# Kernel tuning notes

Hardware: AMD Instinct MI355X
Metric: run time of the kernel (lower is better)

## Reference

```python
import jax, jax.numpy as jnp
import numpy as np

N_NODES = 50000
N_EDGES = 800000
V_IN, V_OUT, E_IN, E_OUT = 128, 64, 64, 64


def setup_inputs() -> dict:
    key = jax.random.key(0)
    ks = jax.random.split(key, 9)
    return {
        "n_feat": jax.random.normal(ks[0], (N_NODES, V_IN), dtype=jnp.float32),
        "e_feat": jax.random.normal(ks[1], (N_EDGES, E_IN), dtype=jnp.float32),
        "src": jax.random.randint(ks[2], (N_EDGES,), 0, N_NODES),
        "dst": jax.random.randint(ks[3], (N_EDGES,), 0, N_NODES),
        "W_a": jax.random.normal(ks[4], (2 * V_IN + E_IN, V_OUT), dtype=jnp.float32) * 0.1,
        "W_T": jax.random.normal(ks[5], (2 * V_IN + E_IN, V_OUT), dtype=jnp.float32) * 0.1,
        "b_T": jnp.zeros((V_OUT,), dtype=jnp.float32),
        "W_e": jax.random.normal(ks[6], (V_IN, E_OUT), dtype=jnp.float32) * 0.1,
        "W_ee": jax.random.normal(ks[7], (E_IN, E_OUT), dtype=jnp.float32) * 0.1,
        "prelu_a": jnp.full((1,), 0.25, dtype=jnp.float32),
    }


def _prelu(x, a):
    return jnp.where(x >= 0, x, a * x)


def reference(n_feat, e_feat, src, dst, W_a, W_T, b_T, W_e, W_ee, prelu_a):
    v, e_in = V_IN, E_IN
    Ns = n_feat[src]            # [E, v_in] gathered source feats
    Nd = n_feat[dst]            # [E, v_in] gathered dest feats
    # concat order in message_function is [N_dst, e, N_src]; split weights instead of
    # materializing the [E, 2v+e] concat.
    Wa_d, Wa_e, Wa_s = W_a[:v], W_a[v:v + e_in], W_a[v + e_in:]
    Wt_d, Wt_e, Wt_s = W_T[:v], W_T[v:v + e_in], W_T[v + e_in:]
    logits = _prelu(Nd @ Wa_d + e_feat @ Wa_e + Ns @ Wa_s, prelu_a)   # [E, v_out]
    unatt = Nd @ Wt_d + e_feat @ Wt_e + Ns @ Wt_s                      # [E, v_out]
    # ragged per-dst-node softmax over incoming-edge mailbox, per feature channel
    m = jax.ops.segment_max(logits, dst, num_segments=N_NODES)         # [N, v_out]
    m = jnp.where(jnp.isfinite(m), m, 0.0)
    ex = jnp.exp(logits - m[dst])                                      # [E, v_out]
    denom = jax.ops.segment_sum(ex, dst, num_segments=N_NODES)         # [N, v_out]
    num = jax.ops.segment_sum(ex * unatt, dst, num_segments=N_NODES)   # [N, v_out]
    deg = jax.ops.segment_sum(jnp.ones((dst.shape[0],), jnp.float32), dst, num_segments=N_NODES)
    has_msg = (deg > 0)[:, None]
    denom_safe = jnp.where(has_msg, denom, 1.0)
    # DGL leaves 0-in-degree nodes at zeros (reduce never called for them)
    new_n_feat = jnp.where(has_msg, num / denom_safe + b_T, 0.0)       # [N, v_out]
    # edge update uses the OLD node features (apply_edges runs before n_feat swap)
    new_e_feat = Ns @ W_e + Nd @ W_e + e_feat @ W_ee                   # [E, e_out]
    return new_n_feat, new_e_feat
```

## Files before the change

### kernel.cpp

```cpp
#include <hip/hip_runtime.h>

#define N_NODES 50000
#define N_EDGES 800000

typedef __attribute__((ext_vector_type(8))) short short8;
typedef __attribute__((ext_vector_type(4))) float f32x4;

__device__ __forceinline__ short bf16_rne(float f) {
  unsigned u = __float_as_uint(f);
  unsigned r = (u + 0x7FFFu + ((u >> 16) & 1u)) >> 16;
  return (short)r;
}

__global__ __launch_bounds__(256) void prep_w(
    const float* __restrict__ W_a, const float* __restrict__ W_T,
    const float* __restrict__ W_e, unsigned short* __restrict__ Wbf) {
  int t = blockIdx.x * 256 + threadIdx.x;
  if (t >= 4 * 20 * 64 * 8) return;
  int kt = t / 10240, rdm = t % 10240;
  int ct = rdm >> 9, L = (rdm >> 3) & 63, j = rdm & 7;
  int k = kt * 32 + (L >> 4) * 8 + j;
  int oc = ct * 16 + (L & 15);
  float v;
  if (oc < 64)       v = W_a[k * 64 + oc];
  else if (oc < 128) v = W_e[k * 64 + (oc - 64)];
  else if (oc < 192) v = W_a[(192 + k) * 64 + (oc - 128)];
  else if (oc < 256) v = W_T[(192 + k) * 64 + (oc - 192)];
  else               v = W_T[k * 64 + (oc - 256)];
  Wbf[t] = (unsigned short)bf16_rne(v);
}

__global__ __launch_bounds__(256) void hist_kernel(
    const int* __restrict__ dst, unsigned* __restrict__ hist) {
  int e = blockIdx.x * 256 + threadIdx.x;
  if (e < N_EDGES) atomicAdd(&hist[dst[e]], 1u);
}

__global__ __launch_bounds__(1024) void scan_cursor(
    const unsigned* __restrict__ hist, unsigned* __restrict__ cursor) {
  __shared__ unsigned sSums[16];
  const int tid = threadIdx.x;
  const int lane = tid & 63;
  const int w = tid >> 6;
  const int CH = (N_NODES + 1023) / 1024;
  const int begin = tid * CH;
  const int end = (begin + CH < N_NODES) ? begin + CH : N_NODES;

  unsigned local = 0;
  for (int i = begin; i < end; ++i) local += hist[i];

  unsigned sum = local;
  #pragma unroll
  for (int off = 1; off < 64; off <<= 1) {
    unsigned t = __shfl_up(sum, off, 64);
    if (lane >= off) sum += t;
  }
  if (lane == 63) sSums[w] = sum;
  __syncthreads();
  if (w == 0) {
    unsigned v = (lane < 16) ? sSums[lane] : 0u;
    unsigned s2 = v;
    #pragma unroll
    for (int off = 1; off < 16; off <<= 1) {
      unsigned t = __shfl_up(s2, off, 64);
      if (lane >= off) s2 += t;
    }
    if (lane < 16) sSums[lane] = s2 - v;
  }
  __syncthreads();

  unsigned run = sSums[w] + (sum - local);
  for (int i = begin; i < end; ++i) {
    cursor[i] = run;
    run += hist[i];
  }
}

__global__ __launch_bounds__(256) void scatter_kernel(
    const int* __restrict__ src, const int* __restrict__ dst,
    unsigned* __restrict__ cursor, int* __restrict__ perm,
    int* __restrict__ ssrc, int* __restrict__ sdst) {
  int e = blockIdx.x * 256 + threadIdx.x;
  if (e >= N_EDGES) return;
  int d = dst[e];
  unsigned pos = atomicAdd(&cursor[d], 1u);
  perm[pos] = e;
  ssrc[pos] = src[e];
  sdst[pos] = d;
}

__global__ __launch_bounds__(256) void node_proj_mfma(
    const float* __restrict__ n_feat, const unsigned short* __restrict__ Wbf,
    uint2* __restrict__ NPs4, float* __restrict__ Ptd) {
  __shared__ short sA[64 * 128];
  const int tid = threadIdx.x;
  const int lane = tid & 63;
  const int wid = tid >> 6;
  const int n0 = blockIdx.x * 64;

  for (int cid = tid; cid < 64 * 16; cid += 256) {
    int nd = cid >> 4, k8 = cid & 15;
    int nsrc = n0 + nd; if (nsrc >= N_NODES) nsrc = N_NODES - 1;
    const float* p = n_feat + (size_t)nsrc * 128 + k8 * 8;
    float4 v0 = *(const float4*)p;
    float4 v1 = *(const float4*)(p + 4);
    short8 a;
    a[0] = bf16_rne(v0.x); a[1] = bf16_rne(v0.y);
    a[2] = bf16_rne(v0.z); a[3] = bf16_rne(v0.w);
    a[4] = bf16_rne(v1.x); a[5] = bf16_rne(v1.y);
    a[6] = bf16_rne(v1.z); a[7] = bf16_rne(v1.w);
    *(short8*)(&sA[nd * 128 + ((k8 ^ (nd & 7)) << 3)]) = a;
  }
  __syncthreads();

  const int row = lane & 15;
  const int q   = lane >> 4;

  short8 afrag[4];
  #pragma unroll
  for (int kt = 0; kt < 4; ++kt) {
    int nd = wid * 16 + row;
    afrag[kt] = *(const short8*)(&sA[nd * 128 + (((kt * 4 + q) ^ (row & 7)) << 3)]);
  }

  const short8* Wb8 = (const short8*)Wbf;
  f32x4 acc[20];
  #pragma unroll
  for (int ct = 0; ct < 20; ++ct) acc[ct] = (f32x4){0.f, 0.f, 0.f, 0.f};
  #pragma unroll
  for (int ct = 0; ct < 20; ++ct)
    #pragma unroll
    for (int kt = 0; kt < 4; ++kt) {
      short8 b = Wb8[(kt * 20 + ct) * 64 + lane];
      acc[ct] = __builtin_amdgcn_mfma_f32_16x16x32_bf16(afrag[kt], b, acc[ct], 0, 0, 0);
    }

  #pragma unroll
  for (int i = 0; i < 4; ++i)
    #pragma unroll
    for (int r = 0; r < 4; ++r) {
      int nd = n0 + wid * 16 + q * 4 + r;
      if (nd < N_NODES) {
        unsigned e16  = (unsigned short)bf16_rne(acc[4  + i][r]);
        unsigned as16 = (unsigned short)bf16_rne(acc[8  + i][r]);
        unsigned ts16 = (unsigned short)bf16_rne(acc[12 + i][r]);
        unsigned ad16 = (unsigned short)bf16_rne(acc[i][r]);
        uint2 v;
        v.x = e16 | (as16 << 16);
        v.y = ts16 | (ad16 << 16);
        NPs4[(size_t)nd * 64 + i * 16 + row] = v;
        Ptd[(size_t)nd * 64 + i * 16 + row] = acc[16 + i][r];
      }
    }
}

__global__ __launch_bounds__(256) void edge_pass_mfma(
    const float* __restrict__ e_feat, const int* __restrict__ perm,
    const int* __restrict__ ssrc, const int* __restrict__ sdst,
    const float* __restrict__ W_a, const float* __restrict__ W_T,
    const float* __restrict__ W_ee, const float* __restrict__ prelu_a,
    const uint2* __restrict__ NPs4,
    float* __restrict__ denom, float* __restrict__ numer,
    float* __restrict__ out_e) {
  __shared__ short sWT[192 * 64];
  __shared__ float sAcc[4][4 * 200];
  const int tid = threadIdx.x;
  const int lane = tid & 63;
  const int wid = tid >> 6;

  for (int idx = tid; idx < 192 * 32; idx += 256) {
    int C = idx >> 5;
    int k = (idx & 31) * 2;
    float f0, f1;
    if (C < 64)       { f0 = W_a[(128 + k) * 64 + C];        f1 = W_a[(129 + k) * 64 + C]; }
    else if (C < 128) { f0 = W_T[(128 + k) * 64 + (C - 64)]; f1 = W_T[(129 + k) * 64 + (C - 64)]; }
    else              { f0 = W_ee[k * 64 + (C - 128)];       f1 = W_ee[(k + 1) * 64 + (C - 128)]; }
    unsigned pack = ((unsigned)(unsigned short)bf16_rne(f0)) |
                    (((unsigned)(unsigned short)bf16_rne(f1)) << 16);
    int sidx = C * 64 + (((k >> 3) ^ (C & 7)) << 3) + (k & 7);
    *(unsigned*)(&sWT[sidx]) = pack;
  }
  __syncthreads();
  const float pa = prelu_a[0];

  const int row = lane & 15;
  const int q   = lane >> 4;
  float* sA = sAcc[wid];

  const int ngroups = N_EDGES / 64;
  for (int g = blockIdx.x; g < ngroups; g += gridDim.x) {
    const int ebase = g * 64 + wid * 16;

    const int sv = ssrc[ebase + row];
    const int dv = sdst[ebase + row];
    const int pv = perm[ebase + row];

    const float* pbase = e_feat + (size_t)pv * 64;
    float4 v00 = *(const float4*)(pbase + q * 8);
    float4 v01 = *(const float4*)(pbase + q * 8 + 4);
    float4 v10 = *(const float4*)(pbase + 32 + q * 8);
    float4 v11 = *(const float4*)(pbase + 32 + q * 8 + 4);

    uint2 ps[16];
    #pragma unroll
    for (int m = 0; m < 16; ++m) {
      int s_m = __builtin_amdgcn_readlane(sv, m);
      ps[m] = NPs4[(size_t)s_m * 64 + lane];
    }

    short8 afrag[2];
    {
      short8 a;
      a[0] = bf16_rne(v00.x); a[1] = bf16_rne(v00.y);
      a[2] = bf16_rne(v00.z); a[3] = bf16_rne(v00.w);
      a[4] = bf16_rne(v01.x); a[5] = bf16_rne(v01.y);
      a[6] = bf16_rne(v01.z); a[7] = bf16_rne(v01.w);
      afrag[0] = a;
      a[0] = bf16_rne(v10.x); a[1] = bf16_rne(v10.y);
      a[2] = bf16_rne(v10.z); a[3] = bf16_rne(v10.w);
      a[4] = bf16_rne(v11.x); a[5] = bf16_rne(v11.y);
      a[6] = bf16_rne(v11.z); a[7] = bf16_rne(v11.w);
      afrag[1] = a;
    }

    f32x4 aa[4], at[4], ae[4];
    #pragma unroll
    for (int ct = 0; ct < 4; ++ct) {
      aa[ct] = (f32x4){0.f, 0.f, 0.f, 0.f};
      at[ct] = (f32x4){0.f, 0.f, 0.f, 0.f};
      ae[ct] = (f32x4){0.f, 0.f, 0.f, 0.f};
    }
    #pragma unroll
    for (int kt = 0; kt < 2; ++kt)
      #pragma unroll
      for (int ct = 0; ct < 4; ++ct) {
        int c = ct * 16 + row;
        int kg = ((kt * 4 + q) ^ (c & 7)) << 3;
        short8 ba = *(const short8*)(&sWT[(c)       * 64 + kg]);
        short8 bt = *(const short8*)(&sWT[(64 + c)  * 64 + kg]);
        short8 be = *(const short8*)(&sWT[(128 + c) * 64 + kg]);
        aa[ct] = __builtin_amdgcn_mfma_f32_16x16x32_bf16(afrag[kt], ba, aa[ct], 0, 0, 0);
        at[ct] = __builtin_amdgcn_mfma_f32_16x16x32_bf16(afrag[kt], bt, at[ct], 0, 0, 0);
        ae[ct] = __builtin_amdgcn_mfma_f32_16x16x32_bf16(afrag[kt], be, ae[ct], 0, 0, 0);
      }

    int dA = -1, dB = -1;
    float dsA = 0.f, nsA = 0.f, eA = 0.f, adA = 0.f;
    float dsB = 0.f, nsB = 0.f, eB = 0.f, adB = 0.f;

    #pragma unroll
    for (int r = 0; r < 4; ++r) {
      #pragma unroll
      for (int ct = 0; ct < 4; ++ct) {
        sA[q * 200 +       ct * 16 + row] = aa[ct][r];
        sA[q * 200 +  64 + ct * 16 + row] = at[ct][r];
        sA[q * 200 + 128 + ct * 16 + row] = ae[ct][r];
      }
      #pragma unroll
      for (int j = 0; j < 4; ++j) {
        const int m = j * 4 + r;
        int d  = __builtin_amdgcn_readlane(dv, m);
        int eo = __builtin_amdgcn_readlane(pv, m);
        float e_s  = __uint_as_float(ps[m].x << 16);
        float as_s = __uint_as_float(ps[m].x & 0xFFFF0000u);
        float ts_s = __uint_as_float(ps[m].y << 16);
        float aaE = sA[j * 200 + lane];
        float atE = sA[j * 200 + 64 + lane];
        float aeE = sA[j * 200 + 128 + lane];

        float e_d, ad_d;
        bool inA;
        if (d == dA) { e_d = eA; ad_d = adA; inA = true; }
        else if (d == dB) { e_d = eB; ad_d = adB; inA = false; }
        else {
          uint2 pdv = NPs4[(size_t)d * 64 + lane];
          e_d  = __uint_as_float(pdv.x << 16);
          ad_d = __uint_as_float(pdv.y & 0xFFFF0000u);
          if (dA < 0) { dA = d; dsA = 0.f; nsA = 0.f; eA = e_d; adA = ad_d; inA = true; }
          else {
            if (dB >= 0) {
              atomicAdd(denom + (size_t)dB * 64 + lane, dsB);
              atomicAdd(numer + (size_t)dB * 64 + lane, nsB);
            }
            dB = d; dsB = 0.f; nsB = 0.f; eB = e_d; adB = ad_d; inA = false;
          }
        }

        float la = ad_d + aaE + as_s;
        float lg = la >= 0.f ? la : pa * la;
        float ex = __expf(lg);
        float exun = ex * (atE + ts_s);
        out_e[(size_t)eo * 64 + lane] = e_s + e_d + aeE;

        if (inA) { dsA += ex; nsA += exun; }
        else     { dsB += ex; nsB += exun; }
      }
    }
    if (dA >= 0) {
      atomicAdd(denom + (size_t)dA * 64 + lane, dsA);
      atomicAdd(numer + (size_t)dA * 64 + lane, nsA);
    }
    if (dB >= 0) {
      atomicAdd(denom + (size_t)dB * 64 + lane, dsB);
      atomicAdd(numer + (size_t)dB * 64 + lane, nsB);
    }
  }
}

__global__ __launch_bounds__(256) void node_final(
    const float* __restrict__ denom, const float* __restrict__ numer,
    const float* __restrict__ Ptd, const float* __restrict__ b_T,
    float* __restrict__ out_n) {
  int t = blockIdx.x * 256 + threadIdx.x;
  if (t >= N_NODES * 64) return;
  float dn = denom[t];
  out_n[t] = dn > 0.f ? numer[t] / dn + Ptd[t] + b_T[t & 63] : 0.f;
}

extern "C" void kernel_launch(void* const* d_in, const int* in_sizes, int n_in,
                              void* d_out, int out_size, void* d_ws, size_t ws_size,
                              hipStream_t stream) {
  const float* n_feat  = (const float*)d_in[0];
  const float* e_feat  = (const float*)d_in[1];
  const int*   src     = (const int*)d_in[2];
  const int*   dst     = (const int*)d_in[3];
  const float* W_a     = (const float*)d_in[4];
  const float* W_T     = (const float*)d_in[5];
  const float* b_T     = (const float*)d_in[6];
  const float* W_e     = (const float*)d_in[7];
  const float* W_ee    = (const float*)d_in[8];
  const float* prelu_a = (const float*)d_in[9];

  float* out_n = (float*)d_out;
  float* out_e = out_n + (size_t)N_NODES * 64;

  uint2* NPs4  = (uint2*)d_ws;
  float* Ptd   = (float*)((char*)d_ws + (size_t)N_NODES * 64 * 8);
  float* denom = Ptd + (size_t)N_NODES * 64;
  float* numer = denom + (size_t)N_NODES * 64;
  unsigned short* Wbf = (unsigned short*)(numer + (size_t)N_NODES * 64);
  unsigned* hist   = (unsigned*)(Wbf + 40960);
  unsigned* cursor = hist + N_NODES;
  int* perm = (int*)(cursor + N_NODES);
  int* ssrc = perm + N_EDGES;
  int* sdst = ssrc + N_EDGES;

  hipMemsetAsync(denom, 0, (size_t)N_NODES * 64 * 2 * sizeof(float), stream);
  hipMemsetAsync(hist, 0, (size_t)N_NODES * sizeof(unsigned), stream);

  prep_w<<<160, 256, 0, stream>>>(W_a, W_T, W_e, Wbf);
  hist_kernel<<<(N_EDGES + 255) / 256, 256, 0, stream>>>(dst, hist);
  scan_cursor<<<1, 1024, 0, stream>>>(hist, cursor);
  scatter_kernel<<<(N_EDGES + 255) / 256, 256, 0, stream>>>(src, dst, cursor,
                                                            perm, ssrc, sdst);
  node_proj_mfma<<<(N_NODES + 63) / 64, 256, 0, stream>>>(n_feat, Wbf, NPs4, Ptd);
  edge_pass_mfma<<<2048, 256, 0, stream>>>(e_feat, perm, ssrc, sdst, W_a, W_T,
                                           W_ee, prelu_a, NPs4, denom, numer, out_e);
  node_final<<<(N_NODES * 64 + 255) / 256, 256, 0, stream>>>(denom, numer, Ptd, b_T, out_n);
}
```

Baseline: 424.4 us.

## Process edges per destination node in CSR order, removing atomics and node_final

The edge pass now iterates per destination node: each wave handles one node's CSR edge range in chunks of 16, accumulates the softmax denominator and numerator in registers, and writes the final node output directly. This removes the denom/numer memset, the float atomics, and the separate node_final kernel. It also merges the histogram and weight-prep kernels and packs src and edge id into one int2 array. In exchange, nodes with degree not divisible by 16 leave MFMA lanes partly idle, and per-wave work varies with node degree, which can cause load imbalance.

```diff
diff --git a/kernel.cpp b/kernel.cpp
--- a/kernel.cpp
+++ b/kernel.cpp
@@ -12,32 +12,34 @@
   return (short)r;
 }
 
-__global__ __launch_bounds__(256) void prep_w(
+__global__ __launch_bounds__(256) void hist_prep(
+    const int* __restrict__ dst, unsigned* __restrict__ hist,
     const float* __restrict__ W_a, const float* __restrict__ W_T,
     const float* __restrict__ W_e, unsigned short* __restrict__ Wbf) {
-  int t = blockIdx.x * 256 + threadIdx.x;
-  if (t >= 4 * 20 * 64 * 8) return;
-  int kt = t / 10240, rdm = t % 10240;
-  int ct = rdm >> 9, L = (rdm >> 3) & 63, j = rdm & 7;
-  int k = kt * 32 + (L >> 4) * 8 + j;
-  int oc = ct * 16 + (L & 15);
-  float v;
-  if (oc < 64)       v = W_a[k * 64 + oc];
-  else if (oc < 128) v = W_e[k * 64 + (oc - 64)];
-  else if (oc < 192) v = W_a[(192 + k) * 64 + (oc - 128)];
-  else if (oc < 256) v = W_T[(192 + k) * 64 + (oc - 192)];
-  else               v = W_T[k * 64 + (oc - 256)];
-  Wbf[t] = (unsigned short)bf16_rne(v);
-}
-
-__global__ __launch_bounds__(256) void hist_kernel(
-    const int* __restrict__ dst, unsigned* __restrict__ hist) {
-  int e = blockIdx.x * 256 + threadIdx.x;
-  if (e < N_EDGES) atomicAdd(&hist[dst[e]], 1u);
+  const int bid = blockIdx.x;
+  if (bid < N_EDGES / 256) {
+    int e = bid * 256 + threadIdx.x;
+    atomicAdd(&hist[dst[e]], 1u);
+  } else {
+    int t = (bid - N_EDGES / 256) * 256 + threadIdx.x;
+    if (t >= 4 * 20 * 64 * 8) return;
+    int kt = t / 10240, rdm = t % 10240;
+    int ct = rdm >> 9, L = (rdm >> 3) & 63, j = rdm & 7;
+    int k = kt * 32 + (L >> 4) * 8 + j;
+    int oc = ct * 16 + (L & 15);
+    float v;
+    if (oc < 64)       v = W_a[k * 64 + oc];
+    else if (oc < 128) v = W_e[k * 64 + (oc - 64)];
+    else if (oc < 192) v = W_a[(192 + k) * 64 + (oc - 128)];
+    else if (oc < 256) v = W_T[(192 + k) * 64 + (oc - 192)];
+    else               v = W_T[k * 64 + (oc - 256)];
+    Wbf[t] = (unsigned short)bf16_rne(v);
+  }
 }
 
 __global__ __launch_bounds__(1024) void scan_cursor(
-    const unsigned* __restrict__ hist, unsigned* __restrict__ cursor) {
+    const unsigned* __restrict__ hist, unsigned* __restrict__ cursor,
+    unsigned* __restrict__ rowptr) {
   __shared__ unsigned sSums[16];
   const int tid = threadIdx.x;
   const int lane = tid & 63;
@@ -72,21 +74,20 @@
   unsigned run = sSums[w] + (sum - local);
   for (int i = begin; i < end; ++i) {
     cursor[i] = run;
+    rowptr[i] = run;
     run += hist[i];
   }
+  if (tid == 0) rowptr[N_NODES] = N_EDGES;
 }
 
 __global__ __launch_bounds__(256) void scatter_kernel(
     const int* __restrict__ src, const int* __restrict__ dst,
-    unsigned* __restrict__ cursor, int* __restrict__ perm,
-    int* __restrict__ ssrc, int* __restrict__ sdst) {
+    unsigned* __restrict__ cursor, int2* __restrict__ se) {
   int e = blockIdx.x * 256 + threadIdx.x;
   if (e >= N_EDGES) return;
   int d = dst[e];
   unsigned pos = atomicAdd(&cursor[d], 1u);
-  perm[pos] = e;
-  ssrc[pos] = src[e];
-  sdst[pos] = d;
+  se[pos] = make_int2(src[e], e);
 }
 
 __global__ __launch_bounds__(256) void node_proj_mfma(
@@ -154,14 +155,14 @@
     }
 }
 
-__global__ __launch_bounds__(256) void edge_pass_mfma(
-    const float* __restrict__ e_feat, const int* __restrict__ perm,
-    const int* __restrict__ ssrc, const int* __restrict__ sdst,
+__global__ __launch_bounds__(256) void edge_node_pass(
+    const float* __restrict__ e_feat, const int2* __restrict__ se,
+    const unsigned* __restrict__ rowptr,
     const float* __restrict__ W_a, const float* __restrict__ W_T,
     const float* __restrict__ W_ee, const float* __restrict__ prelu_a,
-    const uint2* __restrict__ NPs4,
-    float* __restrict__ denom, float* __restrict__ numer,
-    float* __restrict__ out_e) {
+    const uint2* __restrict__ NPs4, const float* __restrict__ Ptd,
+    const float* __restrict__ b_T,
+    float* __restrict__ out_n, float* __restrict__ out_e) {
   __shared__ short sWT[192 * 64];
   __shared__ float sAcc[4][4 * 200];
   const int tid = threadIdx.x;
@@ -182,139 +183,112 @@
   }
   __syncthreads();
   const float pa = prelu_a[0];
+  const float bT = b_T[lane];
 
   const int row = lane & 15;
   const int q   = lane >> 4;
   float* sA = sAcc[wid];
-
-  const int ngroups = N_EDGES / 64;
-  for (int g = blockIdx.x; g < ngroups; g += gridDim.x) {
-    const int ebase = g * 64 + wid * 16;
-
-    const int sv = ssrc[ebase + row];
-    const int dv = sdst[ebase + row];
-    const int pv = perm[ebase + row];
-
-    const float* pbase = e_feat + (size_t)pv * 64;
-    float4 v00 = *(const float4*)(pbase + q * 8);
-    float4 v01 = *(const float4*)(pbase + q * 8 + 4);
-    float4 v10 = *(const float4*)(pbase + 32 + q * 8);
-    float4 v11 = *(const float4*)(pbase + 32 + q * 8 + 4);
-
-    uint2 ps[16];
-    #pragma unroll
-    for (int m = 0; m < 16; ++m) {
-      int s_m = __builtin_amdgcn_readlane(sv, m);
-      ps[m] = NPs4[(size_t)s_m * 64 + lane];
-    }
-
-    short8 afrag[2];
-    {
-      short8 a;
-      a[0] = bf16_rne(v00.x); a[1] = bf16_rne(v00.y);
-      a[2] = bf16_rne(v00.z); a[3] = bf16_rne(v00.w);
-      a[4] = bf16_rne(v01.x); a[5] = bf16_rne(v01.y);
-      a[6] = bf16_rne(v01.z); a[7] = bf16_rne(v01.w);
-      afrag[0] = a;
-      a[0] = bf16_rne(v10.x); a[1] = bf16_rne(v10.y);
-      a[2] = bf16_rne(v10.z); a[3] = bf16_rne(v10.w);
-      a[4] = bf16_rne(v11.x); a[5] = bf16_rne(v11.y);
-      a[6] = bf16_rne(v11.z); a[7] = bf16_rne(v11.w);
-      afrag[1] = a;
-    }
-
-    f32x4 aa[4], at[4], ae[4];
-    #pragma unroll
-    for (int ct = 0; ct < 4; ++ct) {
-      aa[ct] = (f32x4){0.f, 0.f, 0.f, 0.f};
-      at[ct] = (f32x4){0.f, 0.f, 0.f, 0.f};
-      ae[ct] = (f32x4){0.f, 0.f, 0.f, 0.f};
-    }
-    #pragma unroll
-    for (int kt = 0; kt < 2; ++kt)
+  const int nwaves = gridDim.x * 4;
+
+  for (int n = blockIdx.x * 4 + wid; n < N_NODES; n += nwaves) {
+    const unsigned base = rowptr[n];
+    const int deg = (int)(rowptr[n + 1] - base);
+
+    uint2 pdv = NPs4[(size_t)n * 64 + lane];
+    float e_d  = __uint_as_float(pdv.x << 16);
+    float ad_d = __uint_as_float(pdv.y & 0xFFFF0000u);
+
+    float dsum = 0.f, nsum = 0.f;
+
+    for (int b = 0; b < deg; b += 16) {
+      int cnt = deg - b; if (cnt > 16) cnt = 16;
+      int rslot = (int)base + b + (row < cnt ? row : 0);
+      int2 se2 = se[rslot];
+
+      const float* pbase = e_feat + (size_t)se2.y * 64;
+      float4 v00 = *(const float4*)(pbase + q * 8);
+      float4 v01 = *(const float4*)(pbase + q * 8 + 4);
+      float4 v10 = *(const float4*)(pbase + 32 + q * 8);
+      float4 v11 = *(const float4*)(pbase + 32 + q * 8 + 4);
+
+      uint2 ps[16];
+      #pragma unroll
+      for (int m = 0; m < 16; ++m) {
+        if (m < cnt) {
+          int s_m = __builtin_amdgcn_readlane(se2.x, m);
+          ps[m] = NPs4[(size_t)s_m * 64 + lane];
+        }
+      }
+
+      short8 afrag[2];
+      {
+        short8 a;
+        a[0] = bf16_rne(v00.x); a[1] = bf16_rne(v00.y);
+        a[2] = bf16_rne(v00.z); a[3] = bf16_rne(v00.w);
+        a[4] = bf16_rne(v01.x); a[5] = bf16_rne(v01.y);
+        a[6] = bf16_rne(v01.z); a[7] = bf16_rne(v01.w);
+        afrag[0] = a;
+        a[0] = bf16_rne(v10.x); a[1] = bf16_rne(v10.y);
+        a[2] = bf16_rne(v10.z); a[3] = bf16_rne(v10.w);
+        a[4] = bf16_rne(v11.x); a[5] = bf16_rne(v11.y);
+        a[6] = bf16_rne(v11.z); a[7] = bf16_rne(v11.w);
+        afrag[1] = a;
+      }
+
+      f32x4 aa[4], at[4], ae[4];
       #pragma unroll
       for (int ct = 0; ct < 4; ++ct) {
-        int c = ct * 16 + row;
-        int kg = ((kt * 4 + q) ^ (c & 7)) << 3;
-        short8 ba = *(const short8*)(&sWT[(c)       * 64 + kg]);
-        short8 bt = *(const short8*)(&sWT[(64 + c)  * 64 + kg]);
-        short8 be = *(const short8*)(&sWT[(128 + c) * 64 + kg]);
-        aa[ct] = __builtin_amdgcn_mfma_f32_16x16x32_bf16(afrag[kt], ba, aa[ct], 0, 0, 0);
-        at[ct] = __builtin_amdgcn_mfma_f32_16x16x32_bf16(afrag[kt], bt, at[ct], 0, 0, 0);
-        ae[ct] = __builtin_amdgcn_mfma_f32_16x16x32_bf16(afrag[kt], be, ae[ct], 0, 0, 0);
-      }
-
-    int dA = -1, dB = -1;
-    float dsA = 0.f, nsA = 0.f, eA = 0.f, adA = 0.f;
-    float dsB = 0.f, nsB = 0.f, eB = 0.f, adB = 0.f;
-
-    #pragma unroll
-    for (int r = 0; r < 4; ++r) {
+        aa[ct] = (f32x4){0.f, 0.f, 0.f, 0.f};
+        at[ct] = (f32x4){0.f, 0.f, 0.f, 0.f};
+        ae[ct] = (f32x4){0.f, 0.f, 0.f, 0.f};
+      }
       #pragma unroll
-      for (int ct = 0; ct < 4; ++ct) {
-        sA[q * 200 +       ct * 16 + row] = aa[ct][r];
-        sA[q * 200 +  64 + ct * 16 + row] = at[ct][r];
-        sA[q * 200 + 128 + ct * 16 + row] = ae[ct][r];
-      }
+      for (int kt = 0; kt < 2; ++kt)
+        #pragma unroll
+        for (int ct = 0; ct < 4; ++ct) {
+          int c = ct * 16 + row;
+          int kg = ((kt * 4 + q) ^ (c & 7)) << 3;
+          short8 ba = *(const short8*)(&sWT[(c)       * 64 + kg]);
+          short8 bt = *(const short8*)(&sWT[(64 + c)  * 64 + kg]);
+          short8 be = *(const short8*)(&sWT[(128 + c) * 64 + kg]);
+          aa[ct] = __builtin_amdgcn_mfma_f32_16x16x32_bf16(afrag[kt], ba, aa[ct], 0, 0, 0);
+          at[ct] = __builtin_amdgcn_mfma_f32_16x16x32_bf16(afrag[kt], bt, at[ct], 0, 0, 0);
+          ae[ct] = __builtin_amdgcn_mfma_f32_16x16x32_bf16(afrag[kt], be, ae[ct], 0, 0, 0);
+        }
+
       #pragma unroll
-      for (int j = 0; j < 4; ++j) {
-        const int m = j * 4 + r;
-        int d  = __builtin_amdgcn_readlane(dv, m);
-        int eo = __builtin_amdgcn_readlane(pv, m);
-        float e_s  = __uint_as_float(ps[m].x << 16);
-        float as_s = __uint_as_float(ps[m].x & 0xFFFF0000u);
-        float ts_s = __uint_as_float(ps[m].y << 16);
-        float aaE = sA[j * 200 + lane];
-        float atE = sA[j * 200 + 64 + lane];
-        float aeE = sA[j * 200 + 128 + lane];
-
-        float e_d, ad_d;
-        bool inA;
-        if (d == dA) { e_d = eA; ad_d = adA; inA = true; }
-        else if (d == dB) { e_d = eB; ad_d = adB; inA = false; }
-        else {
-          uint2 pdv = NPs4[(size_t)d * 64 + lane];
-          e_d  = __uint_as_float(pdv.x << 16);
-          ad_d = __uint_as_float(pdv.y & 0xFFFF0000u);
-          if (dA < 0) { dA = d; dsA = 0.f; nsA = 0.f; eA = e_d; adA = ad_d; inA = true; }
-          else {
-            if (dB >= 0) {
-              atomicAdd(denom + (size_t)dB * 64 + lane, dsB);
-              atomicAdd(numer + (size_t)dB * 64 + lane, nsB);
-            }
-            dB = d; dsB = 0.f; nsB = 0.f; eB = e_d; adB = ad_d; inA = false;
+      for (int r = 0; r < 4; ++r) {
+        #pragma unroll
+        for (int ct = 0; ct < 4; ++ct) {
+          sA[q * 200 +       ct * 16 + row] = aa[ct][r];
+          sA[q * 200 +  64 + ct * 16 + row] = at[ct][r];
+          sA[q * 200 + 128 + ct * 16 + row] = ae[ct][r];
+        }
+        #pragma unroll
+        for (int j2 = 0; j2 < 4; ++j2) {
+          const int m = j2 * 4 + r;
+          if (m < cnt) {
+            int eo = __builtin_amdgcn_readlane(se2.y, m);
+            float e_s  = __uint_as_float(ps[m].x << 16);
+            float as_s = __uint_as_float(ps[m].x & 0xFFFF0000u);
+            float ts_s = __uint_as_float(ps[m].y << 16);
+            float aaE = sA[j2 * 200 + lane];
+            float atE = sA[j2 * 200 + 64 + lane];
+            float aeE = sA[j2 * 200 + 128 + lane];
+            float la = ad_d + aaE + as_s;
+            float lg = la >= 0.f ? la : pa * la;
+            float ex = __expf(lg);
+            nsum = __builtin_fmaf(ex, atE + ts_s, nsum);
+            dsum += ex;
+            out_e[(size_t)eo * 64 + lane] = e_s + e_d + aeE;
           }
         }
-
-        float la = ad_d + aaE + as_s;
-        float lg = la >= 0.f ? la : pa * la;
-        float ex = __expf(lg);
-        float exun = ex * (atE + ts_s);
-        out_e[(size_t)eo * 64 + lane] = e_s + e_d + aeE;
-
-        if (inA) { dsA += ex; nsA += exun; }
-        else     { dsB += ex; nsB += exun; }
       }
     }
-    if (dA >= 0) {
-      atomicAdd(denom + (size_t)dA * 64 + lane, dsA);
-      atomicAdd(numer + (size_t)dA * 64 + lane, nsA);
-    }
-    if (dB >= 0) {
-      atomicAdd(denom + (size_t)dB * 64 + lane, dsB);
-      atomicAdd(numer + (size_t)dB * 64 + lane, nsB);
-    }
-  }
-}
-
-__global__ __launch_bounds__(256) void node_final(
-    const float* __restrict__ denom, const float* __restrict__ numer,
-    const float* __restrict__ Ptd, const float* __restrict__ b_T,
-    float* __restrict__ out_n) {
-  int t = blockIdx.x * 256 + threadIdx.x;
-  if (t >= N_NODES * 64) return;
-  float dn = denom[t];
-  out_n[t] = dn > 0.f ? numer[t] / dn + Ptd[t] + b_T[t & 63] : 0.f;
+
+    out_n[(size_t)n * 64 + lane] =
+        deg > 0 ? nsum / dsum + Ptd[(size_t)n * 64 + lane] + bT : 0.f;
+  }
 }
 
 extern "C" void kernel_launch(void* const* d_in, const int* in_sizes, int n_in,
@@ -336,25 +310,17 @@
 
   uint2* NPs4  = (uint2*)d_ws;
   float* Ptd   = (float*)((char*)d_ws + (size_t)N_NODES * 64 * 8);
-  float* denom = Ptd + (size_t)N_NODES * 64;
-  float* numer = denom + (size_t)N_NODES * 64;
-  unsigned short* Wbf = (unsigned short*)(numer + (size_t)N_NODES * 64);
+  unsigned short* Wbf = (unsigned short*)(Ptd + (size_t)N_NODES * 64);
   unsigned* hist   = (unsigned*)(Wbf + 40960);
   unsigned* cursor = hist + N_NODES;
-  int* perm = (int*)(cursor + N_NODES);
-  int* ssrc = perm + N_EDGES;
-  int* sdst = ssrc + N_EDGES;
-
-  hipMemsetAsync(denom, 0, (size_t)N_NODES * 64 * 2 * sizeof(float), stream);
+  unsigned* rowptr = cursor + N_NODES;
+  int2* se = (int2*)(rowptr + N_NODES + 2);
+
   hipMemsetAsync(hist, 0, (size_t)N_NODES * sizeof(unsigned), stream);
-
-  prep_w<<<160, 256, 0, stream>>>(W_a, W_T, W_e, Wbf);
-  hist_kernel<<<(N_EDGES + 255) / 256, 256, 0, stream>>>(dst, hist);
-  scan_cursor<<<1, 1024, 0, stream>>>(hist, cursor);
-  scatter_kernel<<<(N_EDGES + 255) / 256, 256, 0, stream>>>(src, dst, cursor,
-                                                            perm, ssrc, sdst);
+  hist_prep<<<N_EDGES / 256 + 160, 256, 0, stream>>>(dst, hist, W_a, W_T, W_e, Wbf);
+  scan_cursor<<<1, 1024, 0, stream>>>(hist, cursor, rowptr);
+  scatter_kernel<<<(N_EDGES + 255) / 256, 256, 0, stream>>>(src, dst, cursor, se);
   node_proj_mfma<<<(N_NODES + 63) / 64, 256, 0, stream>>>(n_feat, Wbf, NPs4, Ptd);
-  edge_pass_mfma<<<2048, 256, 0, stream>>>(e_feat, perm, ssrc, sdst, W_a, W_T,
-                                           W_ee, prelu_a, NPs4, denom, numer, out_e);
-  node_final<<<(N_NODES * 64 + 255) / 256, 256, 0, stream>>>(denom, numer, Ptd, b_T, out_n);
-}
+  edge_node_pass<<<2048, 256, 0, stream>>>(e_feat, se, rowptr, W_a, W_T, W_ee,
+                                           prelu_a, NPs4, Ptd, b_T, out_n, out_e);
+}
```

Result: slower. 447.4 us (+5.4%).
